# Kernel tuning notes

Hardware: AMD Instinct MI355X
Metric: run time of the kernel (lower is better)

The kernel has to match this reference:

```python
import jax, jax.numpy as jnp
import numpy as np

T, N, H, L, C, V = 128, 1024, 256, 64, 64, 1000  # time, batch, hidden, n_lines(=action_n), condition, vocab


def _gru_gates(x, h, Wih, Whh, bih, bhh):
    # PyTorch GRU gate math (gate order: r, z, n)
    gi = x @ Wih.T + bih
    gh = h @ Whh.T + bhh
    ir, iz, i_n = jnp.split(gi, 3, axis=-1)
    hr, hz, h_n = jnp.split(gh, 3, axis=-1)
    r = jax.nn.sigmoid(ir + hr)
    z = jax.nn.sigmoid(iz + hz)
    n = jnp.tanh(i_n + r * h_n)
    return (1.0 - z) * n + z * h


def _gru_scan(xs, Wih, Whh, bih, bhh):
    # xs: [L, N, H] seq-major; zero initial state (matches nn.GRU default)
    h0 = jnp.zeros((xs.shape[1], Whh.shape[1]), dtype=xs.dtype)
    def step(h, x):
        h = _gru_gates(x, h, Wih, Whh, bih, bhh)
        return h, h
    _, ys = jax.lax.scan(step, h0, xs)
    return ys


def setup_inputs() -> dict:
    key = jax.random.key(0)
    ks = jax.random.split(key, 32)
    s = 1.0 / np.sqrt(H)
    u = lambda k, shape: jax.random.uniform(k, shape, jnp.float32, -s, s)
    return {
        "condition": jax.random.normal(ks[0], (T, N, C), jnp.float32),
        "emb": jax.random.normal(ks[1], (V, H), jnp.float32),
        "wih_f": u(ks[2], (3 * H, H)), "whh_f": u(ks[3], (3 * H, H)),
        "bih_f": u(ks[4], (3 * H,)), "bhh_f": u(ks[5], (3 * H,)),
        "wih_b": u(ks[6], (3 * H, H)), "whh_b": u(ks[7], (3 * H, H)),
        "bih_b": u(ks[8], (3 * H,)), "bhh_b": u(ks[9], (3 * H,)),
        "f_w0": u(ks[10], (H, C + H)), "f_b0": u(ks[11], (H,)),
        "f_w1": u(ks[12], (H, H)), "f_b1": u(ks[13], (H,)),
        "c_wih": u(ks[14], (3 * H, H)), "c_whh": u(ks[15], (3 * H, H)),
        "c_bih": u(ks[16], (3 * H,)), "c_bhh": u(ks[17], (3 * H,)),
        "actor_w": u(ks[18], (2 * H, H)), "actor_b": u(ks[19], (2 * H,)),
        "critic_w": u(ks[20], (1, H)), "critic_b": u(ks[21], (1,)),
        "lines": jax.random.randint(ks[22], (N, L), 0, V),
        "actions": jax.random.randint(ks[23], (T, N), 0, L),
    }


def _forward(condition, emb, wih_f, whh_f, bih_f, bhh_f, wih_b, whh_b, bih_b, bhh_b,
             f_w0, f_b0, f_w1, f_b1, c_wih, c_whh, c_bih, c_bhh,
             actor_w, actor_b, critic_w, critic_b, lines, actions):
    M = emb[lines]                           # [N, L, H]
    seq = jnp.transpose(M, (1, 0, 2))        # [L, N, H] seq-major for GRU
    Kf = _gru_scan(seq, wih_f, whh_f, bih_f, bhh_f)
    Kb = _gru_scan(seq[::-1], wih_b, whh_b, bih_b, bhh_b)[::-1]
    K = jnp.transpose(jnp.concatenate([Kf, Kb], -1), (1, 0, 2))  # [N, L, 2H]

    # new episode: rnn_hxs == 0 -> h = 0, p = one_hot(0)
    p0 = jnp.zeros((N, L), M.dtype).at[:, 0].set(1.0)
    h0 = jnp.zeros((N, H), M.dtype)

    def step(carry, inp_t):
        h, p = carry
        cond_t, a_t = inp_t
        r = jnp.einsum('nl,nlh->nh', p, M)                  # pointer read
        x = jnp.concatenate([cond_t, r], -1)
        x = jax.nn.relu(x @ f_w0.T + f_b0)
        x = jax.nn.relu(x @ f_w1.T + f_b1)
        h = _gru_gates(x, h, c_wih, c_whh, c_bih, c_bhh)    # GRUCell
        k = h @ actor_w.T + actor_b                         # [N, 2H]
        w = jnp.einsum('nlh,nh->nl', K, k)                  # logits [N, L]
        a_probs = jax.nn.softmax(w, axis=-1)
        p_new = jax.nn.one_hot(a_t, L, dtype=M.dtype)       # actions all >= 0 -> no sampling
        v = h @ critic_w.T + critic_b                       # [N, 1]
        # pack order per RecurrentState: a, v, h, a_probs, p
        out = jnp.concatenate([a_t[:, None].astype(M.dtype), v, h, a_probs, p_new], -1)
        return (h, p_new), out

    _, hx = jax.lax.scan(step, (h0, p0), (condition, actions))  # hx: [T, N, 1+1+H+L+L]
    return hx


def reference(condition, emb, wih_f, whh_f, bih_f, bhh_f, wih_b, whh_b, bih_b, bhh_b,
              f_w0, f_b0, f_w1, f_b1, c_wih, c_whh, c_bih, c_bhh,
              actor_w, actor_b, critic_w, critic_b, lines, actions):
    hx = _forward(condition, emb, wih_f, whh_f, bih_f, bhh_f, wih_b, whh_b, bih_b, bhh_b,
                  f_w0, f_b0, f_w1, f_b1, c_wih, c_whh, c_bih, c_bhh,
                  actor_w, actor_b, critic_w, critic_b, lines, actions)
    return hx, hx[-1:]
```

## Files before the change

kernel.cpp:

```cpp
#include <hip/hip_runtime.h>


typedef unsigned short u16;
typedef __attribute__((ext_vector_type(8))) short bf16x8;
typedef __attribute__((ext_vector_type(4))) short bf16x4;
typedef __attribute__((ext_vector_type(4))) float f32x4;

#define DEVFN static __device__ __forceinline__

DEVFN float b2f(u16 h){ union{unsigned u; float f;} v; v.u = ((unsigned)h) << 16; return v.f; }
DEVFN u16 f2b(float f){ union{float f; unsigned u;} v; v.f = f;
  return (u16)((v.u + 0x7fffu + ((v.u >> 16) & 1u)) >> 16); }

DEVFN f32x4 mfma16(bf16x8 a, bf16x8 b, f32x4 c){
  asm("v_mfma_f32_16x16x32_bf16 %0, %1, %2, %0" : "+v"(c) : "v"(a), "v"(b));
  return c;
}
DEVFN void gl_lds16(const void* g, void* l){
  __builtin_amdgcn_global_load_lds((const __attribute__((address_space(1))) void*)g,
                                   (__attribute__((address_space(3))) void*)l, 16, 0, 0);
}
DEVFN float sigm(float x){ return __builtin_amdgcn_rcpf(1.0f + __expf(-x)); }
DEVFN float tanhf_(float x){ float e = __expf(2.0f * x); return 1.0f - 2.0f * __builtin_amdgcn_rcpf(e + 1.0f); }


__global__ __launch_bounds__(256) void k_f2b(const float* __restrict__ s, u16* __restrict__ d, int n){
  int i = blockIdx.x * 256 + threadIdx.x;
  if (i < n) d[i] = f2b(s[i]);
}

__global__ __launch_bounds__(256) void k_bias(const float* __restrict__ bih, const float* __restrict__ bhh,
                                              float* __restrict__ dst){
  int i = blockIdx.x * 256 + threadIdx.x;
  if (i < 768) dst[i] = bih[i] + (i < 512 ? bhh[i] : 0.f);
}

template<bool LMAJOR>
__global__ __launch_bounds__(256) void k_embed(const float* __restrict__ emb, const int* __restrict__ lines,
                                               u16* __restrict__ Mh){
  int c = blockIdx.x * 256 + threadIdx.x;
  int row = c >> 5;
  int j = (c & 31) * 8;
  int n, ll;
  if (LMAJOR){ ll = row >> 10; n = row & 1023; } else { n = row >> 6; ll = row & 63; }
  int line = lines[n * 64 + ll];
  const float* s = emb + line * 256 + j;
  bf16x8 v;
  #pragma unroll
  for (int q = 0; q < 8; q++) v[q] = (short)f2b(s[q]);
  *(bf16x8*)&Mh[row * 256 + j] = v;
}

__global__ __launch_bounds__(256) void k_xa(const float* __restrict__ cond, const u16* __restrict__ Mh,
                                            const int* __restrict__ actions, u16* __restrict__ XA){
  int c = blockIdx.x * 256 + threadIdx.x;
  int tn = c / 40;
  int j = (c - tn * 40) * 8;
  bf16x8 v;
  if (j < 64){
    const float* s = cond + tn * 64 + j;
    #pragma unroll
    for (int q = 0; q < 8; q++) v[q] = (short)f2b(s[q]);
  } else {
    int t = tn >> 10, n = tn & 1023;
    int idx = t ? actions[(t - 1) * 1024 + n] : 0;
    v = *(const bf16x8*)&Mh[(n * 64 + idx) * 256 + (j - 64)];
  }
  *(bf16x8*)&XA[tn * 320 + j] = v;
}

template<int MODE, bool BIAS, bool RELU>
__global__ __launch_bounds__(256) void k_gemm(const u16* __restrict__ A, int lda,
                                              const u16* __restrict__ B, int ldb,
                                              const float* __restrict__ bias,
                                              u16* __restrict__ C, int ldc, int K){
  __shared__ __align__(16) u16 sA[4096], sB[4096];
  const int tid = threadIdx.x, wid = tid >> 6, l = tid & 63;
  const int l15 = l & 15, l4 = l >> 4;
  const int bxm = (MODE >= 2) ? blockIdx.y : blockIdx.x;
  const int bxn = (MODE >= 2) ? blockIdx.x : blockIdx.y;
  const int m0 = bxm * 128, n0 = bxn * 128;
  const int wm = (wid >> 1) * 64, wn = (wid & 1) * 64;
  const int srow = wid * 16 + (l >> 2), scol = (l & 3) * 8;
  f32x4 acc[4][4] = {};
  for (int k0 = 0; k0 < K; k0 += 32){
    gl_lds16(&A[(m0 + srow) * lda + k0 + scol],      (char*)sA + wid * 1024);
    gl_lds16(&A[(m0 + 64 + srow) * lda + k0 + scol], (char*)sA + 4096 + wid * 1024);
    gl_lds16(&B[(n0 + srow) * ldb + k0 + scol],      (char*)sB + wid * 1024);
    gl_lds16(&B[(n0 + 64 + srow) * ldb + k0 + scol], (char*)sB + 4096 + wid * 1024);
    __syncthreads();
    bf16x8 af[4], bfr[4];
    #pragma unroll
    for (int i = 0; i < 4; i++) af[i]  = *(const bf16x8*)&sA[(wm + i * 16 + l15) * 32 + l4 * 8];
    #pragma unroll
    for (int j = 0; j < 4; j++) bfr[j] = *(const bf16x8*)&sB[(wn + j * 16 + l15) * 32 + l4 * 8];
    #pragma unroll
    for (int i = 0; i < 4; i++)
      #pragma unroll
      for (int j = 0; j < 4; j++)
        acc[i][j] = mfma16(af[i], bfr[j], acc[i][j]);
    __syncthreads();
  }
  if constexpr (MODE >= 2){
    #pragma unroll
    for (int j = 0; j < 4; j++){
      int colp = wn + j * 16 + l15;
      float bia = BIAS ? bias[n0 + colp] : 0.f;
      size_t cpart = (size_t)blockIdx.x * 2048 + (size_t)(colp >> 4) * 256 + (size_t)(colp & 15) * 4;
      #pragma unroll
      for (int i = 0; i < 4; i++){
        int row = m0 + wm + i * 16 + l4 * 4;
        int t = row >> 10, n = row & 1023;
        size_t addr = ((size_t)t * 64 + (n >> 4)) * 12288 + (size_t)((n >> 2) & 3) * 64 + cpart;
        unsigned q0 = (unsigned)f2b(acc[i][j][0] + bia) | ((unsigned)f2b(acc[i][j][1] + bia) << 16);
        unsigned q1 = (unsigned)f2b(acc[i][j][2] + bia) | ((unsigned)f2b(acc[i][j][3] + bia) << 16);
        uint2 qq; qq.x = q0; qq.y = q1;
        *(uint2*)(C + addr) = qq;
      }
    }
  } else {
    #pragma unroll
    for (int i = 0; i < 4; i++)
      #pragma unroll
      for (int j = 0; j < 4; j++){
        int col = n0 + wn + j * 16 + l15;
        float bia = 0.f;
        if constexpr (BIAS) bia = bias[col];
        #pragma unroll
        for (int r = 0; r < 4; r++){
          int row = m0 + wm + i * 16 + l4 * 4 + r;
          float v = acc[i][j][r] + bia;
          if constexpr (RELU) v = fmaxf(v, 0.f);
          int orow = row;
          if constexpr (MODE == 1) orow = ((row & 1023) << 7) | (row >> 10);
          C[(size_t)orow * ldc + col] = f2b(v);
        }
      }
  }
}


template<bool CELL>
__global__ __launch_bounds__(512) void k_scan(
    const u16* __restrict__ Ga, const u16* __restrict__ Gbk,
    const u16* __restrict__ Wa, const u16* __restrict__ Wb,
    const float* __restrict__ bhha, const float* __restrict__ bhhb,
    u16* __restrict__ Ko, float* __restrict__ out)
{
  const int NSTEP = CELL ? 128 : 64;
  int dir = 0, nb = blockIdx.x;
  const u16 *G = Ga, *W = Wa; const float* bhh = bhha;
  if (!CELL){
    dir = blockIdx.x & 1; nb = blockIdx.x >> 1;
    if (dir){ G = Gbk; W = Wb; bhh = bhhb; }
  }
  const int n0 = nb * 16;
  __shared__ __align__(16) u16 hb[2][16 * 256];
  __shared__ __align__(16) u16 gib[2][12288];
  const int tid = threadIdx.x, wid = tid >> 6, l = tid & 63;
  const int l15 = l & 15, l4 = l >> 4;
  for (int i = tid; i < 4096; i += 512) hb[0][i] = 0;
  const int col0 = wid * 16 + l15, col1 = (wid + 8) * 16 + l15;
  const float bhn0 = bhh[512 + col0], bhn1 = bhh[512 + col1];
  bf16x8 w[3][2][8];
  #pragma unroll
  for (int g = 0; g < 3; g++){
    #pragma unroll
    for (int j = 0; j < 2; j++){
      const u16* wp = W + ((size_t)(g * 256 + (j ? col1 : col0)) * 256 + l4 * 8);
      #pragma unroll
      for (int kt = 0; kt < 8; kt++) w[g][j][kt] = *(const bf16x8*)&wp[kt * 32];
    }
  }
  float h0[4] = {0.f,0.f,0.f,0.f}, h1[4] = {0.f,0.f,0.f,0.f};
  {
    int lc0 = (!CELL && dir) ? 63 : 0;
    const char* src = (const char*)(G + ((size_t)lc0 * 64 + nb) * 12288);
    #pragma unroll
    for (int q = 0; q < 3; q++)
      gl_lds16(src + (wid * 3 + q) * 1024 + l * 16, (char*)&gib[0][(wid * 3 + q) * 512]);
  }
  __syncthreads();
  #pragma unroll 1
  for (int s = 0; s < NSTEP; ++s){
    const int cb = s & 1;
    const int lc = CELL ? s : (dir ? 63 - s : s);
    const int sn = (s + 1 < NSTEP) ? s + 1 : s;
    const int lcn = CELL ? sn : (dir ? 63 - sn : sn);
    {
      const char* src = (const char*)(G + ((size_t)lcn * 64 + nb) * 12288);
      #pragma unroll
      for (int q = 0; q < 3; q++)
        gl_lds16(src + (wid * 3 + q) * 1024 + l * 16, (char*)&gib[cb ^ 1][(wid * 3 + q) * 512]);
    }
    bf16x4 y[6];
    #pragma unroll
    for (int yy = 0; yy < 6; yy++)
      y[yy] = *(const bf16x4*)&gib[cb][yy * 2048 + tid * 4];
    {
      f32x4 a0 = {0,0,0,0}, a1 = {0,0,0,0}, a2 = {0,0,0,0};
      #pragma unroll
      for (int kt = 0; kt < 8; kt++){
        int chunk = (kt * 4 + l4) ^ (l15 & 7);
        bf16x8 af = *(const bf16x8*)&hb[cb][l15 * 256 + chunk * 8];
        a0 = mfma16(af, w[0][0][kt], a0);
        a1 = mfma16(af, w[1][0][kt], a1);
        a2 = mfma16(af, w[2][0][kt], a2);
      }
      #pragma unroll
      for (int r = 0; r < 4; r++){
        int row = l4 * 4 + r;
        float xr = b2f((u16)y[0][r]) + a0[r];
        float xz = b2f((u16)y[2][r]) + a1[r];
        float rg = sigm(xr), zg = sigm(xz);
        float nn = tanhf_(b2f((u16)y[4][r]) + rg * (a2[r] + bhn0));
        float hv = (1.f - zg) * nn + zg * h0[r];
        h0[r] = hv;
        u16 hq = f2b(hv);
        hb[cb ^ 1][row * 256 + ((((col0 >> 3) ^ (row & 7)) << 3) | (col0 & 7))] = hq;
        if (CELL){
          size_t ro = (size_t)lc * 1024 + n0 + row;
          Ko[ro * 256 + col0] = hq;
          out[ro * 386 + 2 + col0] = hv;
        } else {
          Ko[((size_t)(n0 + row) * 64 + lc) * 512 + dir * 256 + col0] = hq;
        }
      }
    }
    {
      f32x4 a0 = {0,0,0,0}, a1 = {0,0,0,0}, a2 = {0,0,0,0};
      #pragma unroll
      for (int kt = 0; kt < 8; kt++){
        int chunk = (kt * 4 + l4) ^ (l15 & 7);
        bf16x8 af = *(const bf16x8*)&hb[cb][l15 * 256 + chunk * 8];
        a0 = mfma16(af, w[0][1][kt], a0);
        a1 = mfma16(af, w[1][1][kt], a1);
        a2 = mfma16(af, w[2][1][kt], a2);
      }
      #pragma unroll
      for (int r = 0; r < 4; r++){
        int row = l4 * 4 + r;
        float xr = b2f((u16)y[1][r]) + a0[r];
        float xz = b2f((u16)y[3][r]) + a1[r];
        float rg = sigm(xr), zg = sigm(xz);
        float nn = tanhf_(b2f((u16)y[5][r]) + rg * (a2[r] + bhn1));
        float hv = (1.f - zg) * nn + zg * h1[r];
        h1[r] = hv;
        u16 hq = f2b(hv);
        hb[cb ^ 1][row * 256 + ((((col1 >> 3) ^ (row & 7)) << 3) | (col1 & 7))] = hq;
        if (CELL){
          size_t ro = (size_t)lc * 1024 + n0 + row;
          Ko[ro * 256 + col1] = hq;
          out[ro * 386 + 2 + col1] = hv;
        } else {
          Ko[((size_t)(n0 + row) * 64 + lc) * 512 + dir * 256 + col1] = hq;
        }
      }
    }
    __syncthreads();
  }
}


__global__ __launch_bounds__(256) void k_logits(const u16* __restrict__ Kc, const u16* __restrict__ kT,
                                                float* __restrict__ out){
  int n = blockIdx.x;
  const int tid = threadIdx.x, wid = tid >> 6, l = tid & 63, l15 = l & 15, l4 = l >> 4;
  const u16* An = kT + n * 65536;
  const u16* Bn = Kc + n * 32768;
  f32x4 acc[2][4] = {};
  for (int kt = 0; kt < 16; ++kt){
    bf16x8 a0 = *(const bf16x8*)&An[(wid * 32 + l15) * 512 + kt * 32 + l4 * 8];
    bf16x8 a1 = *(const bf16x8*)&An[(wid * 32 + 16 + l15) * 512 + kt * 32 + l4 * 8];
    #pragma unroll
    for (int j = 0; j < 4; j++){
      bf16x8 b = *(const bf16x8*)&Bn[(j * 16 + l15) * 512 + kt * 32 + l4 * 8];
      acc[0][j] = mfma16(a0, b, acc[0][j]);
      acc[1][j] = mfma16(a1, b, acc[1][j]);
    }
  }
  #pragma unroll
  for (int i = 0; i < 2; i++)
    #pragma unroll
    for (int r = 0; r < 4; r++){
      float v0 = acc[i][0][r], v1 = acc[i][1][r], v2 = acc[i][2][r], v3 = acc[i][3][r];
      float mx = fmaxf(fmaxf(v0, v1), fmaxf(v2, v3));
      #pragma unroll
      for (int s2 = 1; s2 < 16; s2 <<= 1) mx = fmaxf(mx, __shfl_xor(mx, s2));
      float e0 = __expf(v0 - mx), e1 = __expf(v1 - mx), e2 = __expf(v2 - mx), e3 = __expf(v3 - mx);
      float sm = e0 + e1 + e2 + e3;
      #pragma unroll
      for (int s2 = 1; s2 < 16; s2 <<= 1) sm += __shfl_xor(sm, s2);
      float rs = __builtin_amdgcn_rcpf(sm);
      int t = wid * 32 + i * 16 + l4 * 4 + r;
      float* o = out + (size_t)(t * 1024 + n) * 386 + 258;
      o[l15] = e0 * rs; o[16 + l15] = e1 * rs; o[32 + l15] = e2 * rs; o[48 + l15] = e3 * rs;
    }
}


__global__ __launch_bounds__(256) void k_pack(const int* __restrict__ actions,
                                              const float* __restrict__ cw, const float* __restrict__ cb,
                                              float* __restrict__ out){
  int idx = blockIdx.x * 4 + (threadIdx.x >> 6);
  int l = threadIdx.x & 63;
  float* o = out + (size_t)idx * 386;
  float s = 0.f;
  #pragma unroll
  for (int q = 0; q < 4; q++) s += o[2 + l + q * 64] * cw[l + q * 64];
  #pragma unroll
  for (int m = 32; m; m >>= 1) s += __shfl_down(s, m);
  int a = actions[idx];
  if (l == 0){ o[0] = (float)a; o[1] = s + cb[0]; }
  o[322 + l] = (l == a) ? 1.0f : 0.0f;
}


extern "C" void kernel_launch(void* const* d_in, const int* in_sizes, int n_in,
                              void* d_out, int out_size, void* d_ws, size_t ws_size,
                              hipStream_t stream){
  (void)in_sizes; (void)n_in; (void)out_size; (void)ws_size;
  const float* cond  = (const float*)d_in[0];
  const float* emb   = (const float*)d_in[1];
  const float* wih_f = (const float*)d_in[2];
  const float* whh_f = (const float*)d_in[3];
  const float* bih_f = (const float*)d_in[4];
  const float* bhh_f = (const float*)d_in[5];
  const float* wih_b = (const float*)d_in[6];
  const float* whh_b = (const float*)d_in[7];
  const float* bih_b = (const float*)d_in[8];
  const float* bhh_b = (const float*)d_in[9];
  const float* f_w0  = (const float*)d_in[10];
  const float* f_b0  = (const float*)d_in[11];
  const float* f_w1  = (const float*)d_in[12];
  const float* f_b1  = (const float*)d_in[13];
  const float* c_wih = (const float*)d_in[14];
  const float* c_whh = (const float*)d_in[15];
  const float* c_bih = (const float*)d_in[16];
  const float* c_bhh = (const float*)d_in[17];
  const float* actw  = (const float*)d_in[18];
  const float* actb  = (const float*)d_in[19];
  const float* cw    = (const float*)d_in[20];
  const float* cbi   = (const float*)d_in[21];
  const int* lines   = (const int*)d_in[22];
  const int* actions = (const int*)d_in[23];
  float* out = (float*)d_out;

  char* ws = (char*)d_ws;
  size_t off = 0;
  auto alloc = [&](size_t b){ char* p = ws + off; off += (b + 255) & ~(size_t)255; return p; };
  u16* Mh  = (u16*)alloc((size_t)1024 * 64 * 256 * 2);
  u16* Kc  = (u16*)alloc((size_t)1024 * 64 * 512 * 2);
  char* RA = alloc((size_t)128 * 1024 * 768 * 2);
  char* RD = alloc((size_t)128 * 1024 * 320 * 2);
  u16* X0  = (u16*)alloc((size_t)128 * 1024 * 256 * 2);
  u16* wihf_h = (u16*)alloc(196608 * 2);
  u16* whhf_h = (u16*)alloc(196608 * 2);
  u16* wihb_h = (u16*)alloc(196608 * 2);
  u16* whhb_h = (u16*)alloc(196608 * 2);
  u16* cwih_h = (u16*)alloc(196608 * 2);
  u16* cwhh_h = (u16*)alloc(196608 * 2);
  u16* fw0_h  = (u16*)alloc(81920 * 2);
  u16* fw1_h  = (u16*)alloc(65536 * 2);
  u16* actw_h = (u16*)alloc(131072 * 2);
  float* bc_f = (float*)alloc(768 * 4);
  float* bc_b = (float*)alloc(768 * 4);
  float* bc_c = (float*)alloc(768 * 4);

  u16* Gf  = (u16*)RA;
  u16* Gb  = (u16*)(RA + (size_t)64 * 1024 * 768 * 2);
  u16* GI  = (u16*)RA;
  u16* kT  = (u16*)RA;
  u16* XA  = (u16*)RD;
  u16* X   = (u16*)RD;
  u16* Hh  = (u16*)RD;
  u16* Mh2 = X0;

  const float* srcs[9] = {wih_f, whh_f, wih_b, whh_b, c_wih, c_whh, f_w0, f_w1, actw};
  u16* dsts[9] = {wihf_h, whhf_h, wihb_h, whhb_h, cwih_h, cwhh_h, fw0_h, fw1_h, actw_h};
  const int ns[9] = {196608,196608,196608,196608,196608,196608,81920,65536,131072};
  for (int i = 0; i < 9; i++)
    k_f2b<<<dim3((ns[i] + 255) / 256), dim3(256), 0, stream>>>(srcs[i], dsts[i], ns[i]);
  k_bias<<<dim3(3), dim3(256), 0, stream>>>(bih_f, bhh_f, bc_f);
  k_bias<<<dim3(3), dim3(256), 0, stream>>>(bih_b, bhh_b, bc_b);
  k_bias<<<dim3(3), dim3(256), 0, stream>>>(c_bih, c_bhh, bc_c);
  k_embed<false><<<dim3(8192), dim3(256), 0, stream>>>(emb, lines, Mh);
  k_embed<true ><<<dim3(8192), dim3(256), 0, stream>>>(emb, lines, Mh2);
  k_gemm<2,true,false><<<dim3(6,512), dim3(256), 0, stream>>>(Mh2, 256, wihf_h, 256, bc_f, Gf, 0, 256);
  k_gemm<2,true,false><<<dim3(6,512), dim3(256), 0, stream>>>(Mh2, 256, wihb_h, 256, bc_b, Gb, 0, 256);
  k_scan<false><<<dim3(128), dim3(512), 0, stream>>>(Gf, Gb, whhf_h, whhb_h, bhh_f, bhh_b, Kc, nullptr);
  k_xa<<<dim3(20480), dim3(256), 0, stream>>>(cond, Mh, actions, XA);
  k_gemm<0,true,true><<<dim3(1024,2), dim3(256), 0, stream>>>(XA, 320, fw0_h, 320, f_b0, X0, 256, 320);
  k_gemm<0,true,true><<<dim3(1024,2), dim3(256), 0, stream>>>(X0, 256, fw1_h, 256, f_b1, X, 256, 256);
  k_gemm<2,true,false><<<dim3(6,1024), dim3(256), 0, stream>>>(X, 256, cwih_h, 256, bc_c, GI, 0, 256);
  k_scan<true><<<dim3(64), dim3(512), 0, stream>>>(GI, nullptr, cwhh_h, nullptr, c_bhh, nullptr, Hh, out);
  k_gemm<1,true,false><<<dim3(1024,4), dim3(256), 0, stream>>>(Hh, 256, actw_h, 256, actb, kT, 512, 256);
  k_logits<<<dim3(1024), dim3(256), 0, stream>>>(Kc, kT, out);
  k_pack<<<dim3(32768), dim3(256), 0, stream>>>(actions, cw, cbi, out);
  hipMemcpyAsync(out + (size_t)128 * 1024 * 386, out + (size_t)127 * 1024 * 386,
                 (size_t)1024 * 386 * 4, hipMemcpyDeviceToDevice, stream);
}
```

Before: 1.419 ms.

## Restructure GRU scans: vectorized deferred h stores, merged MFMA, separate fp32 output

The scan kernels no longer write scattered 2-byte bf16 and fp32 hidden-state values to global memory inside the recurrence. Each step instead copies the previous step's swizzled hidden tile from LDS to global memory with 16-byte vector stores, and a new k_hout kernel expands the bf16 hidden states into the fp32 output afterwards. The two MFMA groups are merged so all A fragments are loaded once and six accumulators run together. The __syncthreads is replaced by an explicit waitcnt plus s_barrier, and the duplicate seq-major embedding gather is dropped because k_xa now reads the l-major copy. The trade-off is that the h values in the output are now bf16-rounded instead of fp32, and there is one extra kernel launch.

```diff
diff --git a/kernel.cpp b/kernel.cpp
--- a/kernel.cpp
+++ b/kernel.cpp
@@ -35,14 +35,12 @@
   if (i < 768) dst[i] = bih[i] + (i < 512 ? bhh[i] : 0.f);
 }
 
-template<bool LMAJOR>
 __global__ __launch_bounds__(256) void k_embed(const float* __restrict__ emb, const int* __restrict__ lines,
                                                u16* __restrict__ Mh){
   int c = blockIdx.x * 256 + threadIdx.x;
   int row = c >> 5;
   int j = (c & 31) * 8;
-  int n, ll;
-  if (LMAJOR){ ll = row >> 10; n = row & 1023; } else { n = row >> 6; ll = row & 63; }
+  int ll = row >> 10, n = row & 1023;
   int line = lines[n * 64 + ll];
   const float* s = emb + line * 256 + j;
   bf16x8 v;
@@ -51,7 +49,7 @@
   *(bf16x8*)&Mh[row * 256 + j] = v;
 }
 
-__global__ __launch_bounds__(256) void k_xa(const float* __restrict__ cond, const u16* __restrict__ Mh,
+__global__ __launch_bounds__(256) void k_xa(const float* __restrict__ cond, const u16* __restrict__ Mh2,
                                             const int* __restrict__ actions, u16* __restrict__ XA){
   int c = blockIdx.x * 256 + threadIdx.x;
   int tn = c / 40;
@@ -64,7 +62,7 @@
   } else {
     int t = tn >> 10, n = tn & 1023;
     int idx = t ? actions[(t - 1) * 1024 + n] : 0;
-    v = *(const bf16x8*)&Mh[(n * 64 + idx) * 256 + (j - 64)];
+    v = *(const bf16x8*)&Mh2[((size_t)idx * 1024 + n) * 256 + (j - 64)];
   }
   *(bf16x8*)&XA[tn * 320 + j] = v;
 }
@@ -145,7 +143,7 @@
     const u16* __restrict__ Ga, const u16* __restrict__ Gbk,
     const u16* __restrict__ Wa, const u16* __restrict__ Wb,
     const float* __restrict__ bhha, const float* __restrict__ bhhb,
-    u16* __restrict__ Ko, float* __restrict__ out)
+    u16* __restrict__ Ko)
 {
   const int NSTEP = CELL ? 128 : 64;
   int dir = 0, nb = blockIdx.x;
@@ -155,24 +153,25 @@
     if (dir){ G = Gbk; W = Wb; bhh = bhhb; }
   }
   const int n0 = nb * 16;
-  __shared__ __align__(16) u16 hb[2][16 * 256];
+  __shared__ __align__(16) u16 hb[2][4096];
   __shared__ __align__(16) u16 gib[2][12288];
   const int tid = threadIdx.x, wid = tid >> 6, l = tid & 63;
   const int l15 = l & 15, l4 = l >> 4;
   for (int i = tid; i < 4096; i += 512) hb[0][i] = 0;
-  const int col0 = wid * 16 + l15, col1 = (wid + 8) * 16 + l15;
+  const int col0 = wid * 16 + l15, col1 = col0 + 128;
   const float bhn0 = bhh[512 + col0], bhn1 = bhh[512 + col1];
   bf16x8 w[3][2][8];
   #pragma unroll
-  for (int g = 0; g < 3; g++){
+  for (int g = 0; g < 3; g++)
     #pragma unroll
     for (int j = 0; j < 2; j++){
       const u16* wp = W + ((size_t)(g * 256 + (j ? col1 : col0)) * 256 + l4 * 8);
       #pragma unroll
       for (int kt = 0; kt < 8; kt++) w[g][j][kt] = *(const bf16x8*)&wp[kt * 32];
     }
-  }
   float h0[4] = {0.f,0.f,0.f,0.f}, h1[4] = {0.f,0.f,0.f,0.f};
+  const int orow = tid >> 5, oc8 = tid & 31;
+  const int ocol = ((oc8 ^ (orow & 7)) << 3);
   {
     int lc0 = (!CELL && dir) ? 63 : 0;
     const char* src = (const char*)(G + ((size_t)lc0 * 64 + nb) * 12288);
@@ -181,6 +180,7 @@
       gl_lds16(src + (wid * 3 + q) * 1024 + l * 16, (char*)&gib[0][(wid * 3 + q) * 512]);
   }
   __syncthreads();
+  int lc_prev = 0;
   #pragma unroll 1
   for (int s = 0; s < NSTEP; ++s){
     const int cb = s & 1;
@@ -193,71 +193,82 @@
       for (int q = 0; q < 3; q++)
         gl_lds16(src + (wid * 3 + q) * 1024 + l * 16, (char*)&gib[cb ^ 1][(wid * 3 + q) * 512]);
     }
+    if (s > 0){
+      bf16x8 hv8 = *(const bf16x8*)&hb[cb][tid * 8];
+      if (CELL){
+        *(bf16x8*)&Ko[((size_t)lc_prev * 1024 + n0 + orow) * 256 + ocol] = hv8;
+      } else {
+        *(bf16x8*)&Ko[((size_t)(n0 + orow) * 64 + lc_prev) * 512 + dir * 256 + ocol] = hv8;
+      }
+    }
     bf16x4 y[6];
     #pragma unroll
     for (int yy = 0; yy < 6; yy++)
       y[yy] = *(const bf16x4*)&gib[cb][yy * 2048 + tid * 4];
-    {
-      f32x4 a0 = {0,0,0,0}, a1 = {0,0,0,0}, a2 = {0,0,0,0};
-      #pragma unroll
-      for (int kt = 0; kt < 8; kt++){
-        int chunk = (kt * 4 + l4) ^ (l15 & 7);
-        bf16x8 af = *(const bf16x8*)&hb[cb][l15 * 256 + chunk * 8];
-        a0 = mfma16(af, w[0][0][kt], a0);
-        a1 = mfma16(af, w[1][0][kt], a1);
-        a2 = mfma16(af, w[2][0][kt], a2);
-      }
-      #pragma unroll
-      for (int r = 0; r < 4; r++){
-        int row = l4 * 4 + r;
-        float xr = b2f((u16)y[0][r]) + a0[r];
-        float xz = b2f((u16)y[2][r]) + a1[r];
-        float rg = sigm(xr), zg = sigm(xz);
-        float nn = tanhf_(b2f((u16)y[4][r]) + rg * (a2[r] + bhn0));
-        float hv = (1.f - zg) * nn + zg * h0[r];
-        h0[r] = hv;
-        u16 hq = f2b(hv);
-        hb[cb ^ 1][row * 256 + ((((col0 >> 3) ^ (row & 7)) << 3) | (col0 & 7))] = hq;
-        if (CELL){
-          size_t ro = (size_t)lc * 1024 + n0 + row;
-          Ko[ro * 256 + col0] = hq;
-          out[ro * 386 + 2 + col0] = hv;
-        } else {
-          Ko[((size_t)(n0 + row) * 64 + lc) * 512 + dir * 256 + col0] = hq;
-        }
-      }
-    }
-    {
-      f32x4 a0 = {0,0,0,0}, a1 = {0,0,0,0}, a2 = {0,0,0,0};
-      #pragma unroll
-      for (int kt = 0; kt < 8; kt++){
-        int chunk = (kt * 4 + l4) ^ (l15 & 7);
-        bf16x8 af = *(const bf16x8*)&hb[cb][l15 * 256 + chunk * 8];
-        a0 = mfma16(af, w[0][1][kt], a0);
-        a1 = mfma16(af, w[1][1][kt], a1);
-        a2 = mfma16(af, w[2][1][kt], a2);
-      }
-      #pragma unroll
-      for (int r = 0; r < 4; r++){
-        int row = l4 * 4 + r;
-        float xr = b2f((u16)y[1][r]) + a0[r];
-        float xz = b2f((u16)y[3][r]) + a1[r];
-        float rg = sigm(xr), zg = sigm(xz);
-        float nn = tanhf_(b2f((u16)y[5][r]) + rg * (a2[r] + bhn1));
-        float hv = (1.f - zg) * nn + zg * h1[r];
-        h1[r] = hv;
-        u16 hq = f2b(hv);
-        hb[cb ^ 1][row * 256 + ((((col1 >> 3) ^ (row & 7)) << 3) | (col1 & 7))] = hq;
-        if (CELL){
-          size_t ro = (size_t)lc * 1024 + n0 + row;
-          Ko[ro * 256 + col1] = hq;
-          out[ro * 386 + 2 + col1] = hv;
-        } else {
-          Ko[((size_t)(n0 + row) * 64 + lc) * 512 + dir * 256 + col1] = hq;
-        }
-      }
-    }
-    __syncthreads();
+    bf16x8 af[8];
+    #pragma unroll
+    for (int kt = 0; kt < 8; kt++){
+      int chunk = (kt * 4 + l4) ^ (l15 & 7);
+      af[kt] = *(const bf16x8*)&hb[cb][l15 * 256 + chunk * 8];
+    }
+    f32x4 a00={0,0,0,0}, a10={0,0,0,0}, a20={0,0,0,0};
+    f32x4 a01={0,0,0,0}, a11={0,0,0,0}, a21={0,0,0,0};
+    #pragma unroll
+    for (int kt = 0; kt < 8; kt++){
+      a00 = mfma16(af[kt], w[0][0][kt], a00);
+      a10 = mfma16(af[kt], w[1][0][kt], a10);
+      a20 = mfma16(af[kt], w[2][0][kt], a20);
+      a01 = mfma16(af[kt], w[0][1][kt], a01);
+      a11 = mfma16(af[kt], w[1][1][kt], a11);
+      a21 = mfma16(af[kt], w[2][1][kt], a21);
+    }
+    #pragma unroll
+    for (int r = 0; r < 4; r++){
+      int row = l4 * 4 + r;
+      float rg = sigm(b2f((u16)y[0][r]) + a00[r]);
+      float zg = sigm(b2f((u16)y[2][r]) + a10[r]);
+      float nn = tanhf_(b2f((u16)y[4][r]) + rg * (a20[r] + bhn0));
+      float hv = (1.f - zg) * nn + zg * h0[r];
+      h0[r] = hv;
+      hb[cb ^ 1][row * 256 + ((((col0 >> 3) ^ (row & 7)) << 3) | (col0 & 7))] = f2b(hv);
+    }
+    #pragma unroll
+    for (int r = 0; r < 4; r++){
+      int row = l4 * 4 + r;
+      float rg = sigm(b2f((u16)y[1][r]) + a01[r]);
+      float zg = sigm(b2f((u16)y[3][r]) + a11[r]);
+      float nn = tanhf_(b2f((u16)y[5][r]) + rg * (a21[r] + bhn1));
+      float hv = (1.f - zg) * nn + zg * h1[r];
+      h1[r] = hv;
+      hb[cb ^ 1][row * 256 + ((((col1 >> 3) ^ (row & 7)) << 3) | (col1 & 7))] = f2b(hv);
+    }
+    __builtin_amdgcn_sched_barrier(0);
+    asm volatile("s_waitcnt lgkmcnt(0) vmcnt(1)" ::: "memory");
+    __builtin_amdgcn_sched_barrier(0);
+    __builtin_amdgcn_s_barrier();
+    __builtin_amdgcn_sched_barrier(0);
+    lc_prev = lc;
+  }
+  {
+    bf16x8 hv8 = *(const bf16x8*)&hb[NSTEP & 1][tid * 8];
+    if (CELL){
+      *(bf16x8*)&Ko[((size_t)lc_prev * 1024 + n0 + orow) * 256 + ocol] = hv8;
+    } else {
+      *(bf16x8*)&Ko[((size_t)(n0 + orow) * 64 + lc_prev) * 512 + dir * 256 + ocol] = hv8;
+    }
+  }
+}
+
+
+__global__ __launch_bounds__(256) void k_hout(const u16* __restrict__ Hh, float* __restrict__ out){
+  int c = blockIdx.x * 256 + threadIdx.x;
+  int ro = c >> 5, j = (c & 31) * 8;
+  bf16x8 v = *(const bf16x8*)&Hh[(size_t)ro * 256 + j];
+  float* o = out + (size_t)ro * 386 + 2 + j;
+  #pragma unroll
+  for (int q = 0; q < 4; q++){
+    float2 f; f.x = b2f((u16)v[q * 2]); f.y = b2f((u16)v[q * 2 + 1]);
+    *(float2*)(o + q * 2) = f;
   }
 }
 
@@ -349,7 +360,6 @@
   char* ws = (char*)d_ws;
   size_t off = 0;
   auto alloc = [&](size_t b){ char* p = ws + off; off += (b + 255) & ~(size_t)255; return p; };
-  u16* Mh  = (u16*)alloc((size_t)1024 * 64 * 256 * 2);
   u16* Kc  = (u16*)alloc((size_t)1024 * 64 * 512 * 2);
   char* RA = alloc((size_t)128 * 1024 * 768 * 2);
   char* RD = alloc((size_t)128 * 1024 * 320 * 2);
@@ -384,16 +394,16 @@
   k_bias<<<dim3(3), dim3(256), 0, stream>>>(bih_f, bhh_f, bc_f);
   k_bias<<<dim3(3), dim3(256), 0, stream>>>(bih_b, bhh_b, bc_b);
   k_bias<<<dim3(3), dim3(256), 0, stream>>>(c_bih, c_bhh, bc_c);
-  k_embed<false><<<dim3(8192), dim3(256), 0, stream>>>(emb, lines, Mh);
-  k_embed<true ><<<dim3(8192), dim3(256), 0, stream>>>(emb, lines, Mh2);
+  k_embed<<<dim3(8192), dim3(256), 0, stream>>>(emb, lines, Mh2);
   k_gemm<2,true,false><<<dim3(6,512), dim3(256), 0, stream>>>(Mh2, 256, wihf_h, 256, bc_f, Gf, 0, 256);
   k_gemm<2,true,false><<<dim3(6,512), dim3(256), 0, stream>>>(Mh2, 256, wihb_h, 256, bc_b, Gb, 0, 256);
-  k_scan<false><<<dim3(128), dim3(512), 0, stream>>>(Gf, Gb, whhf_h, whhb_h, bhh_f, bhh_b, Kc, nullptr);
-  k_xa<<<dim3(20480), dim3(256), 0, stream>>>(cond, Mh, actions, XA);
+  k_scan<false><<<dim3(128), dim3(512), 0, stream>>>(Gf, Gb, whhf_h, whhb_h, bhh_f, bhh_b, Kc);
+  k_xa<<<dim3(20480), dim3(256), 0, stream>>>(cond, Mh2, actions, XA);
   k_gemm<0,true,true><<<dim3(1024,2), dim3(256), 0, stream>>>(XA, 320, fw0_h, 320, f_b0, X0, 256, 320);
   k_gemm<0,true,true><<<dim3(1024,2), dim3(256), 0, stream>>>(X0, 256, fw1_h, 256, f_b1, X, 256, 256);
   k_gemm<2,true,false><<<dim3(6,1024), dim3(256), 0, stream>>>(X, 256, cwih_h, 256, bc_c, GI, 0, 256);
-  k_scan<true><<<dim3(64), dim3(512), 0, stream>>>(GI, nullptr, cwhh_h, nullptr, c_bhh, nullptr, Hh, out);
+  k_scan<true><<<dim3(64), dim3(512), 0, stream>>>(GI, nullptr, cwhh_h, nullptr, c_bhh, nullptr, Hh);
+  k_hout<<<dim3(16384), dim3(256), 0, stream>>>(Hh, out);
   k_gemm<1,true,false><<<dim3(1024,4), dim3(256), 0, stream>>>(Hh, 256, actw_h, 256, actb, kT, 512, 256);
   k_logits<<<dim3(1024), dim3(256), 0, stream>>>(Kc, kT, out);
   k_pack<<<dim3(32768), dim3(256), 0, stream>>>(actions, cw, cbi, out);
```

Measured after the change: 1.355 ms. 4.5% less time.
